# Performance work log

Hardware: AMD Instinct MI355X
Metric: run time of the kernel (lower is better)

## Reference

```python
import jax, jax.numpy as jnp
from jax import lax
import numpy as np

B, L, E, K, NCLS = 128, 1024, 8, 3, 5


def conv1d(x, w, b):
    # x: [N,C,L], w: [O,I,3], padding=1 -> same length
    y = lax.conv_general_dilated(x, w, (1,), [(1, 1)], dimension_numbers=('NCH', 'OIH', 'NCH'))
    return y + b[None, :, None]


def maxpool2(x):
    # MaxPool1d(kernel=2, stride=2), floor mode (VALID drops odd tail)
    return lax.reduce_window(x, -jnp.inf, lax.max, (1, 1, 2), (1, 1, 2), 'VALID')


def setup_inputs():
    key = jax.random.key(0)
    ks = jax.random.split(key, 32)
    s = 0.05
    g = lambda i, shp: jax.random.normal(ks[i], shp, jnp.float32) * s
    inp = {}
    inp['x'] = jax.random.normal(ks[0], (B, 1, L), jnp.float32)
    inp['c1_w'], inp['c1_b'] = g(1, (16, 1, 3)), jnp.zeros((16,), jnp.float32)
    # stacked expert conv params (leading dim = E)
    chans = [(16, 16), (16, 32), (32, 64), (64, 128), (128, 256), (256, 512)]
    for j, (ci, co) in enumerate(chans, start=1):
        inp[f'ew{j}'] = g(1 + j, (E, co, ci, 3))
        inp[f'eb{j}'] = jnp.zeros((E, co), jnp.float32)
    inp['r_w'], inp['r_b'] = g(10, (E, 16)), jnp.zeros((E,), jnp.float32)
    inp['c2_w'], inp['c2_b'] = g(11, (1024, 512, 3)), jnp.zeros((1024,), jnp.float32)
    fl = (L // 8 // 2) * 1024
    inp['f1_w'], inp['f1_b'] = g(12, (256, fl)) * 0.2, jnp.zeros((256,), jnp.float32)
    inp['f2_w'], inp['f2_b'] = g(13, (NCLS, 256)), jnp.zeros((NCLS,), jnp.float32)
    return inp


def reference(x, c1_w, c1_b, ew1, eb1, ew2, eb2, ew3, eb3, ew4, eb4, ew5, eb5, ew6, eb6,
              r_w, r_b, c2_w, c2_b, f1_w, f1_b, f2_w, f2_b):
    b = x.shape[0]
    h = jax.nn.relu(conv1d(x, c1_w, c1_b))            # [B,16,L]
    pooled = h.mean(axis=-1)                           # AdaptiveAvgPool1d(1) -> [B,16]
    # (router noise skipped: eval-mode determinism)
    rlogits = pooled @ r_w.T + r_b                     # [B,E]
    probs = jax.nn.softmax(rlogits, axis=-1)
    tg, ti = lax.top_k(probs, K)                       # [B,K]
    tg = tg / tg.sum(axis=-1, keepdims=True)
    gates = jnp.zeros((b, E), probs.dtype).at[jnp.arange(b)[:, None], ti].set(tg)  # dense [B,E]

    def expert(w1, b1, w2, b2, w3, b3, w4, b4, w5, b5, w6, b6):
        y = conv1d(h, w1, b1)
        y = maxpool2(jax.nn.relu(conv1d(y, w2, b2)))   # block1 -> [B,32,L/2]
        y = conv1d(y, w3, b3)
        y = maxpool2(jax.nn.relu(conv1d(y, w4, b4)))   # block2 -> [B,128,L/4]
        y = conv1d(y, w5, b5)
        y = maxpool2(jax.nn.relu(conv1d(y, w6, b6)))   # block3 -> [B,512,L/8]
        return y

    eouts = jax.vmap(expert)(ew1, eb1, ew2, eb2, ew3, eb3, ew4, eb4, ew5, eb5, ew6, eb6)  # [E,B,512,L/8]
    combined = jnp.einsum('be,ebcl->bcl', gates, eouts)  # gated scatter-combine (zero gate == not dispatched)

    y = maxpool2(jax.nn.relu(conv1d(combined, c2_w, c2_b)))  # [B,1024,L/16]
    y = y.reshape(b, -1)
    y = jax.nn.relu(y @ f1_w.T + f1_b)                 # dropout p=0.05 is identity in eval
    out = y @ f2_w.T + f2_b                            # [B,NCLS]

    mean_probs = probs.mean(axis=0)
    cv = jnp.std(mean_probs, ddof=1) / (mean_probs.mean() + 1e-10)  # torch std is unbiased
    return out, cv ** 2
```

## Files before the change

### kernel.cpp

```cpp
#include <hip/hip_runtime.h>
#include <hip/hip_bf16.h>
#include <math.h>

#define B_   128
#define L_   1024
#define E_   8
#define K_   3

typedef float f32x4 __attribute__((ext_vector_type(4)));
typedef short s8v  __attribute__((ext_vector_type(8)));
typedef unsigned short u16x8 __attribute__((ext_vector_type(8)));

__device__ inline ushort f2bf(float v) {
  union { float f; unsigned u; } x; x.f = v;
  unsigned r = (x.u + 0x7fffu + ((x.u >> 16) & 1u)) >> 16;
  return (ushort)r;
}
__device__ inline float bf2f(ushort h) {
  union { unsigned u; float f; } x; x.u = ((unsigned)h) << 16;
  return x.f;
}

__device__ __forceinline__ void gload_lds16(const ushort* g, ushort* l) {
  __builtin_amdgcn_global_load_lds(
      (const __attribute__((address_space(1))) unsigned int*)g,
      (__attribute__((address_space(3))) unsigned int*)l, 16, 0, 0);
}

__global__ __launch_bounds__(256) void conv1_k(
    const float* __restrict__ x, const float* __restrict__ w,
    const float* __restrict__ bias, float* __restrict__ h,
    float* __restrict__ pooled)
{
  const int b = blockIdx.x;
  const int t = threadIdx.x;
  __shared__ float xs[1026];
  __shared__ float wsm[48];
  __shared__ float bs[16];
  __shared__ float red[4][16];

  for (int i = t; i < 1024; i += 256) xs[i + 1] = x[(size_t)b * 1024 + i];
  if (t == 0) { xs[0] = 0.f; xs[1025] = 0.f; }
  if (t < 48) wsm[t] = w[t];
  if (t < 16) bs[t] = bias[t];
  __syncthreads();

  float ps[16];
#pragma unroll
  for (int c = 0; c < 16; ++c) ps[c] = 0.f;

  for (int li = 0; li < 4; ++li) {
    const int l = t + li * 256;
    const float xm = xs[l], x0 = xs[l + 1], xp = xs[l + 2];
#pragma unroll
    for (int co = 0; co < 16; ++co) {
      float v = fmaf(wsm[co * 3 + 0], xm,
                fmaf(wsm[co * 3 + 1], x0,
                fmaf(wsm[co * 3 + 2], xp, bs[co])));
      v = fmaxf(v, 0.f);
      h[((size_t)b * 16 + co) * 1024 + l] = v;
      ps[co] += v;
    }
  }
#pragma unroll
  for (int co = 0; co < 16; ++co) {
    float v = ps[co];
    for (int off = 32; off > 0; off >>= 1) v += __shfl_down(v, off, 64);
    ps[co] = v;
  }
  const int wid = t >> 6, lane = t & 63;
  if (lane == 0) {
#pragma unroll
    for (int co = 0; co < 16; ++co) red[wid][co] = ps[co];
  }
  __syncthreads();
  if (t < 16) pooled[(size_t)b * 16 + t] =
      (red[0][t] + red[1][t] + red[2][t] + red[3][t]) * (1.f / 1024.f);
}

__global__ void router_k(const float* __restrict__ pooled,
                         const float* __restrict__ rw,
                         const float* __restrict__ rb,
                         float* __restrict__ pair_g, int* __restrict__ pair_e,
                         float* __restrict__ cv2_out)
{
  const int b = threadIdx.x;
  __shared__ float pl[128][8];
  __shared__ float mp[8];

  float pv[16];
#pragma unroll
  for (int i = 0; i < 16; ++i) pv[i] = pooled[(size_t)b * 16 + i];

  float lg[8];
#pragma unroll
  for (int e = 0; e < 8; ++e) {
    float s = rb[e];
#pragma unroll
    for (int i = 0; i < 16; ++i) s = fmaf(pv[i], rw[e * 16 + i], s);
    lg[e] = s;
  }
  float mx = lg[0];
#pragma unroll
  for (int e = 1; e < 8; ++e) mx = fmaxf(mx, lg[e]);
  float pr[8]; float sum = 0.f;
#pragma unroll
  for (int e = 0; e < 8; ++e) { pr[e] = expf(lg[e] - mx); sum += pr[e]; }
  const float inv = 1.f / sum;
#pragma unroll
  for (int e = 0; e < 8; ++e) { pr[e] *= inv; pl[b][e] = pr[e]; }

  bool used[8] = {false,false,false,false,false,false,false,false};
  float tg[3]; int ti[3];
  for (int k = 0; k < 3; ++k) {
    float best = -1.f; int bi = 0;
#pragma unroll
    for (int e = 0; e < 8; ++e)
      if (!used[e] && pr[e] > best) { best = pr[e]; bi = e; }
    used[bi] = true; tg[k] = best; ti[k] = bi;
  }
  const float ts = 1.f / (tg[0] + tg[1] + tg[2]);
  for (int k = 0; k < 3; ++k) {
    pair_g[b * 3 + k] = tg[k] * ts;
    pair_e[b * 3 + k] = ti[k];
  }
  __syncthreads();
  if (b < 8) {
    float s = 0.f;
    for (int i = 0; i < 128; ++i) s += pl[i][b];
    mp[b] = s * (1.f / 128.f);
  }
  __syncthreads();
  if (b == 0) {
    float m = 0.f;
    for (int e = 0; e < 8; ++e) m += mp[e];
    m *= (1.f / 8.f);
    float v = 0.f;
    for (int e = 0; e < 8; ++e) { float d = mp[e] - m; v += d * d; }
    v *= (1.f / 7.f);
    const float cv = sqrtf(v) / (m + 1e-10f);
    cv2_out[0] = cv * cv;
  }
}

template <int CI, int CO, int LIN, bool POOL, int CIC, int CO_T, int CO_R,
          int IN_DIV>
__global__ __launch_bounds__(256) void convR_k(
    const float* __restrict__ in, const float* __restrict__ w,
    const float* __restrict__ bias, float* __restrict__ out,
    const int* __restrict__ pe)
{
  constexpr int CQ  = CO_T / CO_R;
  constexpr int LQ  = 256 / CQ;
  constexpr int L_T = LQ * 4;
  constexpr int LOUT = POOL ? (LIN / 2) : LIN;
  constexpr int RS  = L_T + 8;
  constexpr int CG  = CO_R / 4;

  const int p  = blockIdx.x;
  const int cb = blockIdx.y * CO_T;
  const int l0 = blockIdx.z * L_T;
  const int e  = pe ? pe[p] : 0;
  const float* inp = in + (size_t)(p / IN_DIV) * CI * LIN;
  const float* wp  = w + (size_t)e * CO * CI * 3;

  __shared__ float in_s[CIC * RS];
  __shared__ float w_s[CIC * 3 * CO_T];

  const int t  = threadIdx.x;
  const int cq = t / LQ;
  const int lq = t % LQ;

  float acc[CO_R][4];
#pragma unroll
  for (int c = 0; c < CO_R; ++c)
#pragma unroll
    for (int l = 0; l < 4; ++l) acc[c][l] = 0.f;

  for (int c0 = 0; c0 < CI; c0 += CIC) {
    for (int idx = t; idx < CIC * (L_T + 2); idx += 256) {
      const int ci = idx / (L_T + 2);
      const int j  = idx - ci * (L_T + 2);
      const int gl = l0 + j - 1;
      in_s[ci * RS + j] =
          (gl >= 0 && gl < LIN) ? inp[(size_t)(c0 + ci) * LIN + gl] : 0.f;
    }
    for (int i = t; i < CIC * CO_T; i += 256) {
      const int co = i % CO_T;
      const int ci = i / CO_T;
      const float* wsrc = wp + ((size_t)(cb + co) * CI + (c0 + ci)) * 3;
      const float w0 = wsrc[0], w1 = wsrc[1], w2 = wsrc[2];
      w_s[(ci * 3 + 0) * CO_T + co] = w0;
      w_s[(ci * 3 + 1) * CO_T + co] = w1;
      w_s[(ci * 3 + 2) * CO_T + co] = w2;
    }
    __syncthreads();
#pragma unroll 4
    for (int ci = 0; ci < CIC; ++ci) {
      const float* row = &in_s[ci * RS + lq * 4];
      const float4 xa = *reinterpret_cast<const float4*>(row);
      const float2 xb = *reinterpret_cast<const float2*>(row + 4);
      const float xv[6] = {xa.x, xa.y, xa.z, xa.w, xb.x, xb.y};
      const float* wrow = &w_s[ci * 3 * CO_T + cq * CO_R];
#pragma unroll
      for (int k = 0; k < 3; ++k) {
#pragma unroll
        for (int cg = 0; cg < CG; ++cg) {
          const float4 wv =
              *reinterpret_cast<const float4*>(&wrow[k * CO_T + cg * 4]);
          const float wq[4] = {wv.x, wv.y, wv.z, wv.w};
#pragma unroll
          for (int c = 0; c < 4; ++c)
#pragma unroll
            for (int l = 0; l < 4; ++l)
              acc[cg * 4 + c][l] = fmaf(wq[c], xv[l + k], acc[cg * 4 + c][l]);
        }
      }
    }
    __syncthreads();
  }

#pragma unroll
  for (int c = 0; c < CO_R; ++c) {
    const int co = cb + cq * CO_R + c;
    const float bv = bias[(size_t)e * CO + co];
    const float v0 = acc[c][0] + bv, v1 = acc[c][1] + bv;
    const float v2 = acc[c][2] + bv, v3 = acc[c][3] + bv;
    float* op = out + ((size_t)p * CO + co) * LOUT;
    if (POOL) {
      const int lo = (l0 >> 1) + lq * 2;
      float2 r;
      r.x = fmaxf(fmaxf(v0, v1), 0.f);
      r.y = fmaxf(fmaxf(v2, v3), 0.f);
      *reinterpret_cast<float2*>(&op[lo]) = r;
    } else {
      const int l = l0 + lq * 4;
      *reinterpret_cast<float4*>(&op[l]) = make_float4(v0, v1, v2, v3);
    }
  }
}

__global__ void wprep_k(const float* __restrict__ w, ushort* __restrict__ oh,
                        ushort* __restrict__ ol, int E, int CO, int CI,
                        int total)
{
  const int idx = blockIdx.x * 256 + threadIdx.x;
  if (idx >= total) return;
  const int KC = CI >> 5;
  const int j = idx & 31;
  int r = idx >> 5;
  const int co = r % CO; r /= CO;
  const int kc = r % KC; r /= KC;
  const int tp = r % 3;
  const int e  = r / 3;
  const float v = w[(((size_t)e * CO + co) * CI + (kc * 32 + j)) * 3 + tp];
  const ushort hi = f2bf(v);
  oh[idx] = hi;
  ol[idx] = f2bf(v - bf2f(hi));
}

__global__ __launch_bounds__(256) void t0_k(const float* __restrict__ in,
                                            ushort* __restrict__ oh,
                                            ushort* __restrict__ ol)
{
  __shared__ float tile[32][33];
  const int p  = blockIdx.x;
  const int l0 = blockIdx.y * 32;
  const int tx = threadIdx.x & 31;
  const int ty = threadIdx.x >> 5;

#pragma unroll
  for (int i = 0; i < 4; ++i) {
    const int ci = ty + i * 8;
    tile[ci][tx] = in[(size_t)p * 16384 + (size_t)ci * 512 + l0 + tx];
  }
  __syncthreads();
#pragma unroll
  for (int i = 0; i < 4; ++i) {
    const int l = l0 + ty + i * 8;
    const float v = tile[tx][ty + i * 8];
    const size_t o = ((size_t)p * 514 + 1 + l) * 32 + tx;
    const ushort hi = f2bf(v);
    oh[o] = hi;
    ol[o] = f2bf(v - bf2f(hi));
  }
  if (blockIdx.y == 0 && threadIdx.x < 32) {
    const size_t o0 = (size_t)p * 514 * 32 + threadIdx.x;
    const size_t o1 = ((size_t)p * 514 + 513) * 32 + threadIdx.x;
    oh[o0] = 0; ol[o0] = 0; oh[o1] = 0; ol[o1] = 0;
  }
}

__global__ __launch_bounds__(256) void t2_k(const float* __restrict__ comb,
                                            ushort* __restrict__ oh,
                                            ushort* __restrict__ ol)
{
  const size_t o4 = ((size_t)blockIdx.x * 256 + threadIdx.x) * 4;
  const int p = (int)(o4 / 66560);
  const int rem = (int)(o4 - (size_t)p * 66560);
  const int r = rem >> 9;
  const int c = rem & 511;
  ushort4 h4, l4;
  if (r == 0 || r == 129) {
    h4 = make_ushort4(0, 0, 0, 0);
    l4 = make_ushort4(0, 0, 0, 0);
  } else {
    const float4 v =
        *reinterpret_cast<const float4*>(&comb[((size_t)p * 128 + (r - 1)) * 512 + c]);
    h4.x = f2bf(v.x); l4.x = f2bf(v.x - bf2f(h4.x));
    h4.y = f2bf(v.y); l4.y = f2bf(v.y - bf2f(h4.y));
    h4.z = f2bf(v.z); l4.z = f2bf(v.z - bf2f(h4.z));
    h4.w = f2bf(v.w); l4.w = f2bf(v.w - bf2f(h4.w));
  }
  *reinterpret_cast<ushort4*>(&oh[o4]) = h4;
  *reinterpret_cast<ushort4*>(&ol[o4]) = l4;
}

template <int CI, int CO, int L, int OMODE>
__global__ __launch_bounds__(256) void convM_k(
    const ushort* __restrict__ xh, const ushort* __restrict__ xl,
    const ushort* __restrict__ wh, const ushort* __restrict__ wl,
    const float* __restrict__ bias,
    ushort* __restrict__ oh, ushort* __restrict__ ol,
    float* __restrict__ of,
    const int* __restrict__ pe, const float* __restrict__ pg,
    int pair0)
{
  constexpr int KC = CI / 32;
  constexpr int NK = (OMODE == 1) ? 3 : 1;
  const int bx = blockIdx.x;
  const int cb = blockIdx.y * 64;
  const int lz = blockIdx.z * 128;

  __shared__ ushort xs[2][130][32];
  __shared__ ushort wsm[2][3][64][32];
  ushort* xsf = &xs[0][0][0];
  ushort* wsf = &wsm[0][0][0][0];

  const int t = threadIdx.x;
  const int lane = t & 63;
  const int wv = t >> 6;
  const int l16 = lane & 15;
  const int kb8 = (lane >> 4) * 8;

  float gacc[2][4][2];
  if (OMODE == 1) {
#pragma unroll
    for (int a = 0; a < 2; ++a)
#pragma unroll
      for (int b = 0; b < 4; ++b) { gacc[a][b][0] = 0.f; gacc[a][b][1] = 0.f; }
  }

  f32x4 acc[2][4];
  int e = 0; float gate = 1.f; int lp = bx;
  float bv[4];

  for (int kp = 0; kp < NK; ++kp) {
    if (OMODE == 1) {
      const int gp = (pair0 + bx) * 3 + kp;
      e = pe[gp]; gate = pg[gp]; lp = bx * 3 + kp;
    } else if (OMODE == 2) { lp = bx; e = 0; }
    else { lp = bx; e = pe[pair0 + bx]; }

#pragma unroll
    for (int a = 0; a < 2; ++a)
#pragma unroll
      for (int b = 0; b < 4; ++b) acc[a][b] = (f32x4){0.f, 0.f, 0.f, 0.f};

    const size_t xbase = ((size_t)lp * (L + 2) + lz) * CI;

    for (int kc = 0; kc < KC; ++kc) {
      const int c0 = kc * 32;
#pragma unroll
      for (int it = 0; it < 5; ++it) {
        const int g = it * 256 + t;
        if (g < 1040) {
          const int pl = g >= 520;
          const int r = g - pl * 520;
          const int row = r >> 2;
          const int c16 = r & 3;
          const ushort* src =
              (pl ? xl : xh) + xbase + (size_t)row * CI + c0 + c16 * 8;
          gload_lds16(src, xsf + (size_t)g * 8);
        }
      }
#pragma unroll
      for (int it = 0; it < 6; ++it) {
        const int g = it * 256 + t;
        const int pl = g >= 768;
        const int r = g - pl * 768;
        const int tp = r >> 8;
        const int rr = r & 255;
        const int co = rr >> 2;
        const int c16 = rr & 3;
        const ushort* src = (pl ? wl : wh) +
            ((((size_t)e * 3 + tp) * KC + kc) * CO + cb + co) * 32 + c16 * 8;
        gload_lds16(src, wsf + (size_t)g * 8);
      }
      __syncthreads();

#pragma unroll
      for (int tp = 0; tp < 3; ++tp) {
        const int ar = wv * 32 + l16 + tp;
        s8v a00 = *reinterpret_cast<const s8v*>(&xs[0][ar][kb8]);
        s8v a01 = *reinterpret_cast<const s8v*>(&xs[0][ar + 16][kb8]);
        s8v a10 = *reinterpret_cast<const s8v*>(&xs[1][ar][kb8]);
        s8v a11 = *reinterpret_cast<const s8v*>(&xs[1][ar + 16][kb8]);
#pragma unroll
        for (int cs = 0; cs < 4; ++cs) {
          const int brow = cs * 16 + l16;
          s8v bh = *reinterpret_cast<const s8v*>(&wsm[0][tp][brow][kb8]);
          s8v bl = *reinterpret_cast<const s8v*>(&wsm[1][tp][brow][kb8]);
          acc[0][cs] = __builtin_amdgcn_mfma_f32_16x16x32_bf16(a00, bh, acc[0][cs], 0, 0, 0);
          acc[0][cs] = __builtin_amdgcn_mfma_f32_16x16x32_bf16(a00, bl, acc[0][cs], 0, 0, 0);
          acc[0][cs] = __builtin_amdgcn_mfma_f32_16x16x32_bf16(a10, bh, acc[0][cs], 0, 0, 0);
          acc[1][cs] = __builtin_amdgcn_mfma_f32_16x16x32_bf16(a01, bh, acc[1][cs], 0, 0, 0);
          acc[1][cs] = __builtin_amdgcn_mfma_f32_16x16x32_bf16(a01, bl, acc[1][cs], 0, 0, 0);
          acc[1][cs] = __builtin_amdgcn_mfma_f32_16x16x32_bf16(a11, bh, acc[1][cs], 0, 0, 0);
        }
      }
      __syncthreads();
    }

#pragma unroll
    for (int cs = 0; cs < 4; ++cs)
      bv[cs] = bias[(size_t)e * CO + cb + cs * 16 + l16];

    if (OMODE == 1) {
#pragma unroll
      for (int ls = 0; ls < 2; ++ls)
#pragma unroll
        for (int cs = 0; cs < 4; ++cs)
#pragma unroll
          for (int q = 0; q < 2; ++q) {
            const float v0 = acc[ls][cs][q * 2] + bv[cs];
            const float v1 = acc[ls][cs][q * 2 + 1] + bv[cs];
            const float m = fmaxf(fmaxf(v0, v1), 0.f);
            gacc[ls][cs][q] += gate * m;
          }
    }
  }

  if (OMODE == 0) {
#pragma unroll
    for (int ls = 0; ls < 2; ++ls)
#pragma unroll
      for (int cs = 0; cs < 4; ++cs)
#pragma unroll
        for (int r = 0; r < 4; ++r) {
          const int l = lz + wv * 32 + ls * 16 + (lane >> 4) * 4 + r;
          const float v = acc[ls][cs][r] + bv[cs];
          const size_t o = ((size_t)lp * (L + 2) + 1 + l) * CO + cb + cs * 16 + l16;
          const ushort hi = f2bf(v);
          oh[o] = hi;
          ol[o] = f2bf(v - bf2f(hi));
        }
    if (blockIdx.z == 0 && t < 64) {
      const size_t o0 = (size_t)lp * (L + 2) * CO + cb + t;
      const size_t o1 = ((size_t)lp * (L + 2) + (L + 1)) * CO + cb + t;
      oh[o0] = 0; ol[o0] = 0; oh[o1] = 0; ol[o1] = 0;
    }
  } else if (OMODE == 3) {
#pragma unroll
    for (int ls = 0; ls < 2; ++ls)
#pragma unroll
      for (int cs = 0; cs < 4; ++cs)
#pragma unroll
        for (int r = 0; r < 4; r += 2) {
          const float v0 = acc[ls][cs][r] + bv[cs];
          const float v1 = acc[ls][cs][r + 1] + bv[cs];
          const float m = fmaxf(fmaxf(v0, v1), 0.f);
          const int lpp = (lz + wv * 32 + ls * 16 + (lane >> 4) * 4 + r) >> 1;
          const size_t o = ((size_t)lp * (L / 2 + 2) + 1 + lpp) * CO + cb + cs * 16 + l16;
          const ushort hi = f2bf(m);
          oh[o] = hi;
          ol[o] = f2bf(m - bf2f(hi));
        }
    if (blockIdx.z == 0 && t < 64) {
      const size_t o0 = (size_t)lp * (L / 2 + 2) * CO + cb + t;
      const size_t o1 = ((size_t)lp * (L / 2 + 2) + (L / 2 + 1)) * CO + cb + t;
      oh[o0] = 0; ol[o0] = 0; oh[o1] = 0; ol[o1] = 0;
    }
  } else if (OMODE == 1) {
#pragma unroll
    for (int ls = 0; ls < 2; ++ls)
#pragma unroll
      for (int cs = 0; cs < 4; ++cs)
#pragma unroll
        for (int q = 0; q < 2; ++q) {
          const int lpp = (lz + wv * 32 + ls * 16 + (lane >> 4) * 4 + q * 2) >> 1;
          const int co = cb + cs * 16 + l16;
          const size_t o = ((size_t)(pair0 + bx) * (L / 2) + lpp) * CO + co;
          of[o] = gacc[ls][cs][q];
        }
  } else {
#pragma unroll
    for (int ls = 0; ls < 2; ++ls)
#pragma unroll
      for (int cs = 0; cs < 4; ++cs)
#pragma unroll
        for (int r = 0; r < 4; r += 2) {
          const float v0 = acc[ls][cs][r] + bv[cs];
          const float v1 = acc[ls][cs][r + 1] + bv[cs];
          const float m = fmaxf(fmaxf(v0, v1), 0.f);
          const int lpp = (lz + wv * 32 + ls * 16 + (lane >> 4) * 4 + r) >> 1;
          const int co = cb + cs * 16 + l16;
          const size_t o = ((size_t)lp * CO + co) * (L / 2) + lpp;
          of[o] = m;
        }
  }
}

__global__ __launch_bounds__(256) void fc1M_k(const float* __restrict__ X,
                                              const float* __restrict__ W,
                                              float* __restrict__ part)
{
  __shared__ ushort xs[2][128][32];
  __shared__ ushort wsm[2][64][32];
  const int t = threadIdx.x;
  const int lane = t & 63;
  const int wv = t >> 6;
  const int l16 = lane & 15;
  const int kb8 = (lane >> 4) * 8;
  const int ot = blockIdx.x * 64;
  const size_t k0g = (size_t)blockIdx.y * 512;

  f32x4 acc[2][4];
#pragma unroll
  for (int a = 0; a < 2; ++a)
#pragma unroll
    for (int b = 0; b < 4; ++b) acc[a][b] = (f32x4){0.f, 0.f, 0.f, 0.f};

  const int xrow = t >> 1;
  const int xcol = (t & 1) * 16;
  const int wco  = t >> 2;
  const int wk   = (t & 3) * 8;

  for (int it = 0; it < 16; ++it) {
    const size_t k0 = k0g + it * 32;
    {
      const float* src = X + (size_t)xrow * 65536 + k0 + xcol;
      float v[16];
#pragma unroll
      for (int q = 0; q < 4; ++q)
        *reinterpret_cast<float4*>(&v[q * 4]) =
            *reinterpret_cast<const float4*>(src + q * 4);
#pragma unroll
      for (int q = 0; q < 2; ++q) {
        u16x8 hv, lv;
#pragma unroll
        for (int j = 0; j < 8; ++j) {
          const float f = v[q * 8 + j];
          const ushort h = f2bf(f);
          hv[j] = h;
          lv[j] = f2bf(f - bf2f(h));
        }
        *reinterpret_cast<u16x8*>(&xs[0][xrow][xcol + q * 8]) = hv;
        *reinterpret_cast<u16x8*>(&xs[1][xrow][xcol + q * 8]) = lv;
      }
    }
    {
      const float* src = W + (size_t)(ot + wco) * 65536 + k0 + wk;
      float v[8];
      *reinterpret_cast<float4*>(&v[0]) = *reinterpret_cast<const float4*>(src);
      *reinterpret_cast<float4*>(&v[4]) = *reinterpret_cast<const float4*>(src + 4);
      u16x8 hv, lv;
#pragma unroll
      for (int j = 0; j < 8; ++j) {
        const ushort h = f2bf(v[j]);
        hv[j] = h;
        lv[j] = f2bf(v[j] - bf2f(h));
      }
      *reinterpret_cast<u16x8*>(&wsm[0][wco][wk]) = hv;
      *reinterpret_cast<u16x8*>(&wsm[1][wco][wk]) = lv;
    }
    __syncthreads();
#pragma unroll
    for (int ms = 0; ms < 2; ++ms) {
      const int ar = wv * 32 + ms * 16 + l16;
      s8v ah = *reinterpret_cast<const s8v*>(&xs[0][ar][kb8]);
      s8v al = *reinterpret_cast<const s8v*>(&xs[1][ar][kb8]);
#pragma unroll
      for (int cs = 0; cs < 4; ++cs) {
        const int brow = cs * 16 + l16;
        s8v bh = *reinterpret_cast<const s8v*>(&wsm[0][brow][kb8]);
        s8v bl = *reinterpret_cast<const s8v*>(&wsm[1][brow][kb8]);
        acc[ms][cs] = __builtin_amdgcn_mfma_f32_16x16x32_bf16(ah, bh, acc[ms][cs], 0, 0, 0);
        acc[ms][cs] = __builtin_amdgcn_mfma_f32_16x16x32_bf16(ah, bl, acc[ms][cs], 0, 0, 0);
        acc[ms][cs] = __builtin_amdgcn_mfma_f32_16x16x32_bf16(al, bh, acc[ms][cs], 0, 0, 0);
      }
    }
    __syncthreads();
  }

#pragma unroll
  for (int ms = 0; ms < 2; ++ms)
#pragma unroll
    for (int cs = 0; cs < 4; ++cs)
#pragma unroll
      for (int r = 0; r < 4; ++r) {
        const int row = wv * 32 + ms * 16 + (lane >> 4) * 4 + r;
        const int col = ot + cs * 16 + l16;
        part[((size_t)blockIdx.y * 128 + row) * 256 + col] = acc[ms][cs][r];
      }
}

__global__ void fc1red_k(const float* __restrict__ part,
                         const float* __restrict__ b1, float* __restrict__ o1)
{
  const int idx = blockIdx.x * 256 + threadIdx.x;
  if (idx < 32768) {
    float s = 0.f;
#pragma unroll 8
    for (int z = 0; z < 128; ++z) s += part[(size_t)z * 32768 + idx];
    o1[idx] = fmaxf(s + b1[idx & 255], 0.f);
  }
}

__global__ void fc2_k(const float* __restrict__ o1, const float* __restrict__ w2,
                      const float* __restrict__ b2, float* __restrict__ out)
{
  const int b = blockIdx.x;
  const int lane = threadIdx.x;
  float acc[5] = {0.f, 0.f, 0.f, 0.f, 0.f};
  for (int i = lane; i < 256; i += 64) {
    const float xv = o1[(size_t)b * 256 + i];
#pragma unroll
    for (int o = 0; o < 5; ++o) acc[o] = fmaf(xv, w2[o * 256 + i], acc[o]);
  }
#pragma unroll
  for (int o = 0; o < 5; ++o) {
    for (int off = 32; off > 0; off >>= 1)
      acc[o] += __shfl_down(acc[o], off, 64);
  }
  if (lane == 0) {
#pragma unroll
    for (int o = 0; o < 5; ++o) out[b * 5 + o] = acc[o] + b2[o];
  }
}

extern "C" void kernel_launch(void* const* d_in, const int* in_sizes, int n_in,
                              void* d_out, int out_size, void* d_ws,
                              size_t ws_size, hipStream_t stream)
{
  const float* x   = (const float*)d_in[0];
  const float* c1w = (const float*)d_in[1];
  const float* c1b = (const float*)d_in[2];
  const float* ew[6];
  const float* eb[6];
  for (int j = 0; j < 6; ++j) {
    ew[j] = (const float*)d_in[3 + 2 * j];
    eb[j] = (const float*)d_in[4 + 2 * j];
  }
  const float* rw  = (const float*)d_in[15];
  const float* rb  = (const float*)d_in[16];
  const float* c2w = (const float*)d_in[17];
  const float* c2b = (const float*)d_in[18];
  const float* f1w = (const float*)d_in[19];
  const float* f1b = (const float*)d_in[20];
  const float* f2w = (const float*)d_in[21];
  const float* f2b = (const float*)d_in[22];
  float* out = (float*)d_out;

  const int chunkB = (ws_size >= 108000000ull) ? 32 : 16;
  const int chunkP = chunkB * 3;
  const int nchunk = 128 / chunkB;

  char* basep = (char*)d_ws;
  size_t off = 0;
  auto alloc = [&](size_t bytes) -> void* {
    off = (off + 255) & ~(size_t)255;
    void* r = basep + off;
    off += bytes;
    return r;
  };

  float* h      = (float*)alloc(2097152ull * 4);
  float* pooled = (float*)alloc(2048ull * 4);
  float* pairg  = (float*)alloc(384ull * 4);
  int*   paire  = (int*)  alloc(384ull * 4);
  float* fc1o   = (float*)alloc(32768ull * 4);
  float* comb   = (float*)alloc(8388608ull * 4);

  const size_t chunk_base = (off + 255) & ~(size_t)255;
  const size_t sA = (size_t)chunkP * 33024 * 2 * 2;
  const size_t sB = (size_t)chunkP * 66048 * 2 * 2;
  const size_t creg = (sA + sB + 511 > 68157440ull) ? (sA + sB + 511)
                                                    : 68157440ull;
  char* slotA = (char*)alloc(sA);
  char* slotB = (char*)alloc(sB);
  if (creg > sA + sB + 511) off = chunk_base + creg;

  float*  bufA  = (float*)slotA;
  ushort* xt3h  = (ushort*)slotA;
  ushort* xt3l  = xt3h + (size_t)chunkP * 16448;
  ushort* xt5h  = (ushort*)slotA;
  ushort* xt5l  = xt5h + (size_t)chunkP * 33024;
  float*  bufB  = (float*)slotB;
  ushort* yE3h  = (ushort*)slotB;
  ushort* yE3l  = yE3h + (size_t)chunkP * 32896;
  ushort* y5h   = (ushort*)slotB;
  ushort* y5l   = y5h + (size_t)chunkP * 66048;

  ushort* xtFh  = (ushort*)(basep + chunk_base);
  ushort* xtFl  = xtFh + 8519680ull;
  float*  part  = (float*)(basep + chunk_base);

  ushort* wp3h  = (ushort*)alloc(49152ull * 2);
  ushort* wp3l  = (ushort*)alloc(49152ull * 2);
  ushort* wp4h  = (ushort*)alloc(196608ull * 2);
  ushort* wp4l  = (ushort*)alloc(196608ull * 2);
  ushort* wp5h  = (ushort*)alloc(786432ull * 2);
  ushort* wp5l  = (ushort*)alloc(786432ull * 2);
  ushort* wp6h  = (ushort*)alloc(3145728ull * 2);
  ushort* wp6l  = (ushort*)alloc(3145728ull * 2);
  ushort* wpFh  = (ushort*)alloc(1572864ull * 2);
  ushort* wpFl  = (ushort*)alloc(1572864ull * 2);

  conv1_k<<<128, 256, 0, stream>>>(x, c1w, c1b, h, pooled);
  router_k<<<1, 128, 0, stream>>>(pooled, rw, rb, pairg, paire, out + 640);

  wprep_k<<<(49152 + 255) / 256, 256, 0, stream>>>(ew[2], wp3h, wp3l, 8, 64, 32, 49152);
  wprep_k<<<(196608 + 255) / 256, 256, 0, stream>>>(ew[3], wp4h, wp4l, 8, 128, 64, 196608);
  wprep_k<<<(786432 + 255) / 256, 256, 0, stream>>>(ew[4], wp5h, wp5l, 8, 256, 128, 786432);
  wprep_k<<<(3145728 + 255) / 256, 256, 0, stream>>>(ew[5], wp6h, wp6l, 8, 512, 256, 3145728);
  wprep_k<<<(1572864 + 255) / 256, 256, 0, stream>>>(c2w, wpFh, wpFl, 1, 1024, 512, 1572864);

  for (int c = 0; c < nchunk; ++c) {
    const int b0 = c * chunkB;
    const int p0 = c * chunkP;
    convR_k<16, 16, 1024, false, 16, 16, 4, 3>
        <<<dim3(chunkP, 1, 4), 256, 0, stream>>>(
            h + (size_t)b0 * 16 * 1024, ew[0], eb[0], bufA, paire + p0);
    convR_k<16, 32, 1024, true, 16, 32, 8, 1>
        <<<dim3(chunkP, 1, 4), 256, 0, stream>>>(bufA, ew[1], eb[1], bufB,
                                                 paire + p0);
    t0_k<<<dim3(chunkP, 16), 256, 0, stream>>>(bufB, xt3h, xt3l);
    convM_k<32, 64, 512, 0>
        <<<dim3(chunkP, 1, 4), 256, 0, stream>>>(xt3h, xt3l, wp3h, wp3l, eb[2],
                                                 yE3h, yE3l, nullptr, paire,
                                                 nullptr, p0);
    convM_k<64, 128, 512, 3>
        <<<dim3(chunkP, 2, 4), 256, 0, stream>>>(yE3h, yE3l, wp4h, wp4l, eb[3],
                                                 xt5h, xt5l, nullptr, paire,
                                                 nullptr, p0);
    convM_k<128, 256, 256, 0>
        <<<dim3(chunkP, 4, 2), 256, 0, stream>>>(xt5h, xt5l, wp5h, wp5l, eb[4],
                                                 y5h, y5l, nullptr, paire,
                                                 nullptr, p0);
    convM_k<256, 512, 256, 1>
        <<<dim3(chunkB, 8, 2), 256, 0, stream>>>(y5h, y5l, wp6h, wp6l, eb[5],
                                                 nullptr, nullptr, comb,
                                                 paire, pairg, b0);
  }

  t2_k<<<8320, 256, 0, stream>>>(comb, xtFh, xtFl);
  convM_k<512, 1024, 128, 2>
      <<<dim3(128, 16, 1), 256, 0, stream>>>(xtFh, xtFl, wpFh, wpFl, c2b,
                                             nullptr, nullptr, comb, nullptr,
                                             nullptr, 0);

  fc1M_k<<<dim3(4, 128), 256, 0, stream>>>(comb, f1w, part);
  fc1red_k<<<128, 256, 0, stream>>>(part, f1b, fc1o);
  fc2_k<<<128, 64, 0, stream>>>(fc1o, f2w, f2b, out);
}
```

Before: 665.3 us.

## Fuse combined-output bf16 split into expert conv6 epilogue and raise MFMA priority

The last expert conv now writes the gated combine directly as padded hi/lo bf16 pairs, so the separate t2_k conversion kernel and the fp32 round trip through comb are removed. Workspace layout is reorganised so that xtF gets its own allocation and comb aliases the per-chunk slots, and chunkB is fixed at 32 regardless of workspace size. s_setprio is raised around the MFMA loops in convM_k and the fc1 kernel so that waves doing matrix math are favoured over waves issuing loads. The risks are that the aliasing of comb with the slot buffers and the fixed chunk size must fit the provided workspace.

Measured after the change: 645.3 us. 1.03x faster.

```diff
diff --git a/kernel.cpp b/kernel.cpp
--- a/kernel.cpp
+++ b/kernel.cpp
@@ -291,31 +291,6 @@
   }
 }
 
-__global__ __launch_bounds__(256) void t2_k(const float* __restrict__ comb,
-                                            ushort* __restrict__ oh,
-                                            ushort* __restrict__ ol)
-{
-  const size_t o4 = ((size_t)blockIdx.x * 256 + threadIdx.x) * 4;
-  const int p = (int)(o4 / 66560);
-  const int rem = (int)(o4 - (size_t)p * 66560);
-  const int r = rem >> 9;
-  const int c = rem & 511;
-  ushort4 h4, l4;
-  if (r == 0 || r == 129) {
-    h4 = make_ushort4(0, 0, 0, 0);
-    l4 = make_ushort4(0, 0, 0, 0);
-  } else {
-    const float4 v =
-        *reinterpret_cast<const float4*>(&comb[((size_t)p * 128 + (r - 1)) * 512 + c]);
-    h4.x = f2bf(v.x); l4.x = f2bf(v.x - bf2f(h4.x));
-    h4.y = f2bf(v.y); l4.y = f2bf(v.y - bf2f(h4.y));
-    h4.z = f2bf(v.z); l4.z = f2bf(v.z - bf2f(h4.z));
-    h4.w = f2bf(v.w); l4.w = f2bf(v.w - bf2f(h4.w));
-  }
-  *reinterpret_cast<ushort4*>(&oh[o4]) = h4;
-  *reinterpret_cast<ushort4*>(&ol[o4]) = l4;
-}
-
 template <int CI, int CO, int L, int OMODE>
 __global__ __launch_bounds__(256) void convM_k(
     const ushort* __restrict__ xh, const ushort* __restrict__ xl,
@@ -399,6 +374,7 @@
       }
       __syncthreads();
 
+      __builtin_amdgcn_s_setprio(1);
 #pragma unroll
       for (int tp = 0; tp < 3; ++tp) {
         const int ar = wv * 32 + l16 + tp;
@@ -419,6 +395,7 @@
           acc[1][cs] = __builtin_amdgcn_mfma_f32_16x16x32_bf16(a11, bh, acc[1][cs], 0, 0, 0);
         }
       }
+      __builtin_amdgcn_s_setprio(0);
       __syncthreads();
     }
 
@@ -490,9 +467,19 @@
         for (int q = 0; q < 2; ++q) {
           const int lpp = (lz + wv * 32 + ls * 16 + (lane >> 4) * 4 + q * 2) >> 1;
           const int co = cb + cs * 16 + l16;
-          const size_t o = ((size_t)(pair0 + bx) * (L / 2) + lpp) * CO + co;
-          of[o] = gacc[ls][cs][q];
+          const size_t o =
+              ((size_t)(pair0 + bx) * (L / 2 + 2) + 1 + lpp) * CO + co;
+          const float g = gacc[ls][cs][q];
+          const ushort hi = f2bf(g);
+          oh[o] = hi;
+          ol[o] = f2bf(g - bf2f(hi));
         }
+    if (blockIdx.z == 0 && t < 64) {
+      const size_t o0 = (size_t)(pair0 + bx) * (L / 2 + 2) * CO + cb + t;
+      const size_t o1 =
+          ((size_t)(pair0 + bx) * (L / 2 + 2) + (L / 2 + 1)) * CO + cb + t;
+      oh[o0] = 0; ol[o0] = 0; oh[o1] = 0; ol[o1] = 0;
+    }
   } else {
 #pragma unroll
     for (int ls = 0; ls < 2; ++ls)
@@ -575,6 +562,7 @@
       *reinterpret_cast<u16x8*>(&wsm[1][wco][wk]) = lv;
     }
     __syncthreads();
+    __builtin_amdgcn_s_setprio(1);
 #pragma unroll
     for (int ms = 0; ms < 2; ++ms) {
       const int ar = wv * 32 + ms * 16 + l16;
@@ -590,6 +578,7 @@
         acc[ms][cs] = __builtin_amdgcn_mfma_f32_16x16x32_bf16(al, bh, acc[ms][cs], 0, 0, 0);
       }
     }
+    __builtin_amdgcn_s_setprio(0);
     __syncthreads();
   }
 
@@ -662,7 +651,7 @@
   const float* f2b = (const float*)d_in[22];
   float* out = (float*)d_out;
 
-  const int chunkB = (ws_size >= 108000000ull) ? 32 : 16;
+  const int chunkB = 32;
   const int chunkP = chunkB * 3;
   const int nchunk = 128 / chunkB;
 
@@ -680,16 +669,15 @@
   float* pairg  = (float*)alloc(384ull * 4);
   int*   paire  = (int*)  alloc(384ull * 4);
   float* fc1o   = (float*)alloc(32768ull * 4);
-  float* comb   = (float*)alloc(8388608ull * 4);
-
-  const size_t chunk_base = (off + 255) & ~(size_t)255;
-  const size_t sA = (size_t)chunkP * 33024 * 2 * 2;
-  const size_t sB = (size_t)chunkP * 66048 * 2 * 2;
-  const size_t creg = (sA + sB + 511 > 68157440ull) ? (sA + sB + 511)
-                                                    : 68157440ull;
-  char* slotA = (char*)alloc(sA);
-  char* slotB = (char*)alloc(sB);
-  if (creg > sA + sB + 511) off = chunk_base + creg;
+
+  ushort* xtFh  = (ushort*)alloc(8519680ull * 2 * 2);
+  ushort* xtFl  = xtFh + 8519680ull;
+  float*  part  = (float*)xtFh;
+
+  const size_t slot_base = (off + 255) & ~(size_t)255;
+  char* slotA = (char*)alloc((size_t)chunkP * 33024 * 2 * 2);
+  char* slotB = (char*)alloc((size_t)chunkP * 66048 * 2 * 2);
+  float* comb = (float*)(basep + slot_base);
 
   float*  bufA  = (float*)slotA;
   ushort* xt3h  = (ushort*)slotA;
@@ -701,10 +689,6 @@
   ushort* yE3l  = yE3h + (size_t)chunkP * 32896;
   ushort* y5h   = (ushort*)slotB;
   ushort* y5l   = y5h + (size_t)chunkP * 66048;
-
-  ushort* xtFh  = (ushort*)(basep + chunk_base);
-  ushort* xtFl  = xtFh + 8519680ull;
-  float*  part  = (float*)(basep + chunk_base);
 
   ushort* wp3h  = (ushort*)alloc(49152ull * 2);
   ushort* wp3l  = (ushort*)alloc(49152ull * 2);
@@ -750,11 +734,10 @@
                                                  nullptr, p0);
     convM_k<256, 512, 256, 1>
         <<<dim3(chunkB, 8, 2), 256, 0, stream>>>(y5h, y5l, wp6h, wp6l, eb[5],
-                                                 nullptr, nullptr, comb,
+                                                 xtFh, xtFl, nullptr,
                                                  paire, pairg, b0);
   }
 
-  t2_k<<<8320, 256, 0, stream>>>(comb, xtFh, xtFl);
   convM_k<512, 1024, 128, 2>
       <<<dim3(128, 16, 1), 256, 0, stream>>>(xtFh, xtFl, wpFh, wpFl, c2b,
                                              nullptr, nullptr, comb, nullptr,
```
